# Performance work log

Hardware: AMD Instinct MI355X
Metric: run time of the kernel (lower is better)

The kernel has to match this reference:

```python
import jax, jax.numpy as jnp
import numpy as np

P, G, UV = 5, 40000, 256          # n_parts, gs_num (visible UV texels), uv_size
ZD, FD, HD = 32, 64, 32           # latent_z_dim, latent_f_dim, latent_h_dim
H1, L1 = 128, 3                   # mlp1 hidden dim, fc layers
H2, L2 = 128, 3                   # mlp2 hidden dim, fc layers
CC, LC = 64, 4                    # cnn hidden channels, cnn hidden layers


def _mlp_params(key, din, hid, nlayers, dout, nparts):
    ks = jax.random.split(key, 3)
    s = lambda f: 1.0 / np.sqrt(f)
    return dict(
        w_in=jax.random.normal(ks[0], (nparts, din, hid), jnp.float32) * s(din),
        b_in=jnp.zeros((nparts, hid), jnp.float32),
        w_hid=jax.random.normal(ks[1], (nparts, nlayers - 1, hid, hid), jnp.float32) * s(hid),
        b_hid=jnp.zeros((nparts, nlayers - 1, hid), jnp.float32),
        w_out=jax.random.normal(ks[2], (nparts, hid, dout), jnp.float32) * s(hid),
        b_out=jnp.zeros((nparts, dout), jnp.float32),
    )


def setup_inputs() -> dict:
    key = jax.random.key(0)
    ks = jax.random.split(key, 12)
    d1 = FD + ZD
    d2 = d1 + 3 + 11
    inp = {
        'latent_z': jax.random.normal(ks[2], (G, ZD), jnp.float32),
        'latent_f': jax.random.normal(ks[3], (P, FD), jnp.float32),
        'cano_xyz': jax.random.normal(ks[4], (G, 3), jnp.float32),
    }
    for k, v in _mlp_params(ks[0], d1, H1, L1, 11, P).items():
        inp['mlp1_' + k] = v
    for k, v in _mlp_params(ks[1], d2, H2, L2, HD, P).items():
        inp['mlp2_' + k] = v
    inp['conv_in_w'] = jax.random.normal(ks[5], (CC, HD, 3, 3), jnp.float32) * (1.0 / np.sqrt(HD * 9))
    inp['conv_in_b'] = jnp.zeros((CC,), jnp.float32)
    inp['conv_hid_w'] = jax.random.normal(ks[6], (LC - 1, CC, CC, 3, 3), jnp.float32) * (1.0 / np.sqrt(CC * 9))
    inp['conv_hid_b'] = jnp.zeros((LC - 1, CC), jnp.float32)
    inp['conv_out_w'] = jax.random.normal(ks[7], (3, CC, 3, 3), jnp.float32) * (1.0 / np.sqrt(CC * 9))
    inp['conv_out_b'] = jnp.zeros((3,), jnp.float32)
    inp['gs_part'] = jax.random.randint(ks[8], (G,), 0, P, jnp.int32)
    inp['uv_idx'] = jax.random.permutation(ks[9], UV * UV)[:G].astype(jnp.int32)  # unique visible texels
    return inp


def _part_mlp(x, w_in, b_in, w_hid, b_hid, w_out, b_out, part):
    # x: [G, D]; weights stacked over parts. Run every part's MLP, gather by part id.
    h = jax.nn.leaky_relu(jnp.einsum('gd,pdh->pgh', x, w_in) + b_in[:, None, :])
    for l in range(w_hid.shape[1]):
        h = jax.nn.leaky_relu(jnp.einsum('pgh,pho->pgo', h, w_hid[:, l]) + b_hid[:, l][:, None, :])
    out = jnp.einsum('pgh,pho->pgo', h, w_out) + b_out[:, None, :]  # [P, G, O]
    return out[part, jnp.arange(out.shape[1])]                       # [G, O]


def _conv(x, w, b):
    y = jax.lax.conv_general_dilated(x, w, (1, 1), 'SAME',
                                     dimension_numbers=('NCHW', 'OIHW', 'NCHW'))
    return y + b[None, :, None, None]


def _instance_norm(x, eps=1e-5):
    m = x.mean(axis=(2, 3), keepdims=True)
    v = x.var(axis=(2, 3), keepdims=True)
    return (x - m) / jnp.sqrt(v + eps)


def reference(latent_z, latent_f, cano_xyz,
              mlp1_w_in, mlp1_b_in, mlp1_w_hid, mlp1_b_hid, mlp1_w_out, mlp1_b_out,
              mlp2_w_in, mlp2_b_in, mlp2_w_hid, mlp2_b_hid, mlp2_w_out, mlp2_b_out,
              conv_in_w, conv_in_b, conv_hid_w, conv_hid_b, conv_out_w, conv_out_b,
              gs_part, uv_idx):
    feat_f = latent_f[gs_part]                                  # [G, FD] per-part feature gather
    x1 = jnp.concatenate([feat_f, latent_z], axis=-1)           # [G, FD+ZD]
    attrs = _part_mlp(x1, mlp1_w_in, mlp1_b_in, mlp1_w_hid, mlp1_b_hid,
                      mlp1_w_out, mlp1_b_out, gs_part)          # [G, 11] gaussian attrs
    x2 = jnp.concatenate([x1, cano_xyz, attrs], axis=-1)        # [G, FD+ZD+3+11]
    h = _part_mlp(x2, mlp2_w_in, mlp2_b_in, mlp2_w_hid, mlp2_b_hid,
                  mlp2_w_out, mlp2_b_out, gs_part)              # [G, HD]
    # scatter per-gaussian features back into the UV map (uvmask-indexed texels)
    uvmap = jnp.zeros((UV * UV, h.shape[-1]), h.dtype).at[uv_idx].add(h)
    x = uvmap.T.reshape(1, h.shape[-1], UV, UV)                 # [1, HD, UV, UV]
    # CNN refinement: conv -> (relu, conv, instance_norm) x (LC-1) -> conv -> sigmoid
    x = _conv(x, conv_in_w, conv_in_b)
    for l in range(conv_hid_w.shape[0]):
        x = _instance_norm(_conv(jax.nn.relu(x), conv_hid_w[l], conv_hid_b[l]))
    x = _conv(x, conv_out_w, conv_out_b)
    return jax.nn.sigmoid(x)                                    # [1, 3, UV, UV]
```

## Files before the change

kernel.cpp:

```cpp
#include <hip/hip_runtime.h>

#define G_N 40000
#define P_N 5
#define PIX 65536
#define XP 136
#define SP 40

typedef short short8 __attribute__((ext_vector_type(8)));
typedef short short4v __attribute__((ext_vector_type(4)));
typedef float f32x4 __attribute__((ext_vector_type(4)));
#define MFMA16(a, b, c) __builtin_amdgcn_mfma_f32_16x16x32_bf16(a, b, c, 0, 0, 0)

__device__ __forceinline__ short f2b(float f) {
    unsigned u = __builtin_bit_cast(unsigned, f);
    unsigned r = (u + 0x7fffu + ((u >> 16) & 1u)) >> 16;
    return (short)r;
}
__device__ __forceinline__ float b2f(short s) {
    unsigned u = ((unsigned)(unsigned short)s) << 16;
    return __builtin_bit_cast(float, u);
}


__global__ __launch_bounds__(256) void hist_k(const int* __restrict__ part,
                                              int* __restrict__ counts, int n) {
    __shared__ int s_c[P_N];
    if (threadIdx.x < P_N) s_c[threadIdx.x] = 0;
    __syncthreads();
    int g = blockIdx.x * 256 + threadIdx.x;
    if (g < n) atomicAdd(&s_c[part[g]], 1);
    __syncthreads();
    if (threadIdx.x < P_N) atomicAdd(&counts[threadIdx.x], s_c[threadIdx.x]);
}

__global__ void offs_k(const int* __restrict__ counts, int* __restrict__ offs) {
    if (threadIdx.x == 0) {
        int o = 0;
        for (int p = 0; p < P_N; ++p) {
            offs[p] = o;
            o += (counts[p] + 63) & ~63;
        }
        offs[P_N] = o;
    }
}

__global__ __launch_bounds__(256) void scatter_k(const int* __restrict__ part,
                                                 const int* __restrict__ offs,
                                                 int* __restrict__ cursors,
                                                 int* __restrict__ perm, int n) {
    const int t = threadIdx.x;
    const int g = blockIdx.x * 256 + t;
    const int p = (g < n) ? part[g] : -1;
    const int lane = t & 63;
    const int wid = t >> 6;
    __shared__ int s_wc[4][P_N];
    __shared__ int s_base[P_N];
    const unsigned long long lmask = (1ull << lane) - 1ull;
    int myrank = 0;
    for (int pp = 0; pp < P_N; ++pp) {
        unsigned long long m = __ballot(p == pp);
        if (p == pp) myrank = __popcll(m & lmask);
        if (lane == 0) s_wc[wid][pp] = __popcll(m);
    }
    __syncthreads();
    if (t < P_N) {
        int tot = s_wc[0][t] + s_wc[1][t] + s_wc[2][t] + s_wc[3][t];
        s_base[t] = atomicAdd(&cursors[t], tot);
    }
    __syncthreads();
    if (g < n) {
        int pre = 0;
        #pragma unroll
        for (int w2 = 0; w2 < 4; ++w2) if (w2 < wid) pre += s_wc[w2][p];
        perm[offs[p] + s_base[p] + pre + myrank] = g;
    }
}


__device__ __forceinline__ float mseg(int l, const float* __restrict__ src,
                                      int DIN, int DOUT, int NP, int pps) {
    const int pn = NP * 128;
    const int p = l / pn;
    const int r = l - p * pn;
    const int n = r >> 7, k = r & 127;
    return (n < DOUT && k < DIN) ? src[p * pps + k * DOUT + n] : 0.f;
}
__device__ __forceinline__ float cseg(int l, const float* __restrict__ src, int CIN) {
    const int per = 9 * 64 * CIN;
    const int ll = l / per;
    int rem = l - ll * per;
    const int tap = rem / (64 * CIN);
    rem -= tap * 64 * CIN;
    const int och = rem / CIN;
    const int ci = rem - och * CIN;
    return src[((ll * 64 + och) * CIN + ci) * 9 + tap];
}

__global__ __launch_bounds__(256) void prep_k(
        const float* __restrict__ m1wi, const float* __restrict__ m1wh,
        const float* __restrict__ m1wo, const float* __restrict__ m2wi,
        const float* __restrict__ m2wh, const float* __restrict__ m2wo,
        const float* __restrict__ cinw, const float* __restrict__ chw,
        short* __restrict__ wb) {
    const int idx = blockIdx.x * 256 + threadIdx.x;
    if (idx >= 651264) return;
    float v;
    if      (idx < 81920)  v = mseg(idx,          m1wi,         96, 128, 128, 12288);
    else if (idx < 163840) v = mseg(idx - 81920,  m1wh,        128, 128, 128, 32768);
    else if (idx < 245760) v = mseg(idx - 163840, m1wh + 16384,128, 128, 128, 32768);
    else if (idx < 256000) v = mseg(idx - 245760, m1wo,        128,  11,  16, 1408);
    else if (idx < 337920) v = mseg(idx - 256000, m2wi,        110, 128, 128, 14080);
    else if (idx < 419840) v = mseg(idx - 337920, m2wh,        128, 128, 128, 32768);
    else if (idx < 501760) v = mseg(idx - 419840, m2wh + 16384,128, 128, 128, 32768);
    else if (idx < 522240) v = mseg(idx - 501760, m2wo,        128,  32,  32, 4096);
    else if (idx < 540672) v = cseg(idx - 522240, cinw, 32);
    else                   v = cseg(idx - 540672, chw, 64);
    wb[idx] = f2b(v);
}


template<int NKC, bool ACT>
__device__ __forceinline__ void wcompute(const short8 (&A)[4][NKC],
                                         const short* __restrict__ wt,
                                         const float* __restrict__ bias,
                                         short* dst) {
    const int ln = threadIdx.x & 15, lq = threadIdx.x >> 4;
    #pragma unroll
    for (int nt = 0; nt < 8; ++nt) {
        short8 B[NKC];
        #pragma unroll
        for (int kc = 0; kc < NKC; ++kc)
            B[kc] = *(const short8*)(wt + (nt * 16 + ln) * 128 + kc * 32 + lq * 8);
        const float bs = bias[nt * 16 + ln];
        #pragma unroll
        for (int mt = 0; mt < 4; ++mt) {
            f32x4 acc = {bs, bs, bs, bs};
            #pragma unroll
            for (int kc = 0; kc < NKC; ++kc) acc = MFMA16(A[mt][kc], B[kc], acc);
            #pragma unroll
            for (int r = 0; r < 4; ++r) {
                float v = acc[r];
                if (ACT) v = fmaxf(v, 0.01f * v);
                dst[(mt * 16 + lq * 4 + r) * XP + nt * 16 + ln] = f2b(v);
            }
        }
    }
}

__device__ __forceinline__ void preload4(short8 (&A)[4][4], const short* s) {
    const int ln = threadIdx.x & 15, lq = threadIdx.x >> 4;
    #pragma unroll
    for (int mt = 0; mt < 4; ++mt)
        #pragma unroll
        for (int kc = 0; kc < 4; ++kc)
            A[mt][kc] = *(const short8*)(s + (mt * 16 + ln) * XP + kc * 32 + lq * 8);
}

__global__ __launch_bounds__(64, 2) void mlp_k(
        const float* __restrict__ latent_z, const float* __restrict__ latent_f,
        const float* __restrict__ cano,
        const short* __restrict__ wt1i, const float* __restrict__ b1i,
        const short* __restrict__ wt1h0, const short* __restrict__ wt1h1,
        const float* __restrict__ b1h,
        const short* __restrict__ wt1o, const float* __restrict__ b1o,
        const short* __restrict__ wt2i, const float* __restrict__ b2i,
        const short* __restrict__ wt2h0, const short* __restrict__ wt2h1,
        const float* __restrict__ b2h,
        const short* __restrict__ wt2o, const float* __restrict__ b2o,
        const int* __restrict__ uv_idx, const int* __restrict__ perm,
        const int* __restrict__ offs, const int* __restrict__ counts,
        unsigned short* __restrict__ uvmap ) {
    __shared__ short s_h[64 * XP];
    __shared__ short s_c4[64 * SP];
    __shared__ int s_g[64];
    __shared__ int s_uv[64];

    const int t = threadIdx.x;
    const int ln = t & 15, lq = t >> 4;
    const int pos0 = blockIdx.x * 64;
    if (pos0 >= offs[P_N]) return;
    int p = 0;
    #pragma unroll
    for (int q = 1; q < P_N; ++q) if (pos0 >= offs[q]) p = q;
    const int vend = offs[p] + counts[p];

    {
        const int pos = pos0 + t;
        const int g = (pos < vend) ? perm[pos] : -1;
        s_g[t] = g;
        s_uv[t] = (g >= 0) ? uv_idx[g] : 0;
    }
    for (int i = t; i < 64 * SP / 2; i += 64) ((int*)s_c4)[i] = 0;
    __syncthreads();

    for (int i = t; i < 64 * 16; i += 64) {
        const int g = i >> 4, k4 = (i & 15) * 4;
        const float4 v = *(const float4*)(latent_f + p * 64 + k4);
        short4v o = {f2b(v.x), f2b(v.y), f2b(v.z), f2b(v.w)};
        *(short4v*)(s_h + g * XP + k4) = o;
    }
    for (int i = t; i < 64 * 8; i += 64) {
        const int g = i >> 3, k4 = (i & 7) * 4;
        const int gg = s_g[g];
        short4v o = {0, 0, 0, 0};
        if (gg >= 0) {
            const float4 v = *(const float4*)(latent_z + gg * 32 + k4);
            o[0] = f2b(v.x); o[1] = f2b(v.y); o[2] = f2b(v.z); o[3] = f2b(v.w);
        }
        *(short4v*)(s_h + g * XP + 64 + k4) = o;
    }
    for (int i = t; i < 64 * 3; i += 64) {
        const int g = i / 3, k = i - g * 3;
        const int gg = s_g[g];
        s_c4[g * SP + k] = (gg >= 0) ? f2b(cano[gg * 3 + k]) : 0;
    }
    __syncthreads();

    short8 A1[4][3];
    #pragma unroll
    for (int mt = 0; mt < 4; ++mt)
        #pragma unroll
        for (int kc = 0; kc < 3; ++kc)
            A1[mt][kc] = *(const short8*)(s_h + (mt * 16 + ln) * XP + kc * 32 + lq * 8);
    __syncthreads();

    wcompute<3, true>(A1, wt1i + p * 16384, b1i + p * 128, s_h);
    __syncthreads();
    {
        short8 Ah[4][4];
        preload4(Ah, s_h); __syncthreads();
        wcompute<4, true>(Ah, wt1h0 + p * 16384, b1h + (p * 2 + 0) * 128, s_h);
        __syncthreads();
        preload4(Ah, s_h); __syncthreads();
        wcompute<4, true>(Ah, wt1h1 + p * 16384, b1h + (p * 2 + 1) * 128, s_h);
        __syncthreads();
        preload4(Ah, s_h); __syncthreads();
        short8 B[4];
        #pragma unroll
        for (int kc = 0; kc < 4; ++kc)
            B[kc] = *(const short8*)(wt1o + p * 2048 + ln * 128 + kc * 32 + lq * 8);
        const float bs = (ln < 11) ? b1o[p * 11 + ln] : 0.f;
        #pragma unroll
        for (int mt = 0; mt < 4; ++mt) {
            f32x4 acc = {bs, bs, bs, bs};
            #pragma unroll
            for (int kc = 0; kc < 4; ++kc) acc = MFMA16(Ah[mt][kc], B[kc], acc);
            if (ln < 11) {
                #pragma unroll
                for (int r = 0; r < 4; ++r)
                    s_c4[(mt * 16 + lq * 4 + r) * SP + 3 + ln] = f2b(acc[r]);
            }
        }
    }
    __syncthreads();

    {
        short8 A2[4][4];
        #pragma unroll
        for (int mt = 0; mt < 4; ++mt) {
            A2[mt][0] = A1[mt][0]; A2[mt][1] = A1[mt][1]; A2[mt][2] = A1[mt][2];
            A2[mt][3] = *(const short8*)(s_c4 + (mt * 16 + ln) * SP + lq * 8);
        }
        __syncthreads();
        wcompute<4, true>(A2, wt2i + p * 16384, b2i + p * 128, s_h);
    }
    __syncthreads();
    {
        short8 Ah[4][4];
        preload4(Ah, s_h); __syncthreads();
        wcompute<4, true>(Ah, wt2h0 + p * 16384, b2h + (p * 2 + 0) * 128, s_h);
        __syncthreads();
        preload4(Ah, s_h); __syncthreads();
        wcompute<4, true>(Ah, wt2h1 + p * 16384, b2h + (p * 2 + 1) * 128, s_h);
        __syncthreads();
        preload4(Ah, s_h);
        #pragma unroll
        for (int nt = 0; nt < 2; ++nt) {
            short8 B[4];
            #pragma unroll
            for (int kc = 0; kc < 4; ++kc)
                B[kc] = *(const short8*)(wt2o + p * 4096 + (nt * 16 + ln) * 128 + kc * 32 + lq * 8);
            const float bs = b2o[p * 32 + nt * 16 + ln];
            #pragma unroll
            for (int mt = 0; mt < 4; ++mt) {
                f32x4 acc = {bs, bs, bs, bs};
                #pragma unroll
                for (int kc = 0; kc < 4; ++kc) acc = MFMA16(Ah[mt][kc], B[kc], acc);
                #pragma unroll
                for (int r = 0; r < 4; ++r) {
                    const int m = mt * 16 + lq * 4 + r;
                    const int g = s_g[m];
                    if (g >= 0)
                        uvmap[s_uv[m] * 32 + nt * 16 + ln] = (unsigned short)f2b(acc[r]);
                }
            }
        }
    }
}


template<int CIN, int TRANS, bool STATS>
__global__ __launch_bounds__(128, 2) void conv_k(
        const unsigned short* __restrict__ in,
        const short* __restrict__ wt,
        const float* __restrict__ bias,
        const float* __restrict__ psum, const float* __restrict__ psq,
        unsigned short* __restrict__ out,
        float* __restrict__ ssum, float* __restrict__ ssq) {
    constexpr int CS = CIN + 8;
    constexpr int NKC = CIN / 32;
    constexpr int RUNS = CIN / 8;
    __shared__ short s_in[10 * 18 * CS];
    __shared__ float s_mr[2][64];
    __shared__ float s_red[2][2][64];

    const int t = threadIdx.x;
    const int ln = t & 15, lq = (t >> 4) & 3;
    const int w2 = t >> 6;
    const int tx0 = blockIdx.x * 16, ty0 = blockIdx.y * 8;

    if (TRANS == 2 && t < 64) {
        const float m = psum[t] * (1.f / PIX);
        const float vv = psq[t] * (1.f / PIX) - m * m;
        s_mr[0][t] = m;
        s_mr[1][t] = rsqrtf(vv + 1e-5f);
    }
    if (TRANS == 2) __syncthreads();

    for (int i = t; i < 180 * RUNS; i += 128) {
        const int sp = i / RUNS, run = i - sp * RUNS;
        const int r = sp / 18, c = sp - r * 18;
        const int gy = ty0 + r - 1, gx = tx0 + c - 1;
        short* dst = &s_in[(r * 18 + c) * CS + run * 8];
        if (gy >= 0 && gy < 256 && gx >= 0 && gx < 256) {
            short8 v = *(const short8*)(in + ((gy * 256 + gx) * CIN + run * 8));
            if (TRANS == 0) {
                *(short8*)dst = v;
            } else {
                short8 o;
                #pragma unroll
                for (int j = 0; j < 8; ++j) {
                    float f = b2f(v[j]);
                    if (TRANS == 2) f = (f - s_mr[0][run * 8 + j]) * s_mr[1][run * 8 + j];
                    o[j] = f2b(fmaxf(f, 0.f));
                }
                *(short8*)dst = o;
            }
        } else {
            short8 z = {0, 0, 0, 0, 0, 0, 0, 0};
            *(short8*)dst = z;
        }
    }
    __syncthreads();

    f32x4 acc[4][4];
    {
        float bs[4];
        #pragma unroll
        for (int nt = 0; nt < 4; ++nt) bs[nt] = bias[nt * 16 + ln];
        #pragma unroll
        for (int mt = 0; mt < 4; ++mt)
            #pragma unroll
            for (int nt = 0; nt < 4; ++nt) {
                f32x4 a = {bs[nt], bs[nt], bs[nt], bs[nt]};
                acc[mt][nt] = a;
            }
    }

    #pragma unroll
    for (int tap = 0; tap < 9; ++tap) {
        const int dy = tap / 3, dx = tap - dy * 3;
        const short* wtap = wt + tap * 64 * CIN;
        #pragma unroll
        for (int kc = 0; kc < NKC; ++kc) {
            short8 B[4];
            #pragma unroll
            for (int nt = 0; nt < 4; ++nt)
                B[nt] = *(const short8*)(wtap + (nt * 16 + ln) * CIN + kc * 32 + lq * 8);
            short8 A[4];
            #pragma unroll
            for (int mt = 0; mt < 4; ++mt)
                A[mt] = *(const short8*)&s_in[((w2 * 4 + mt + dy) * 18 + ln + dx) * CS + kc * 32 + lq * 8];
            #pragma unroll
            for (int mt = 0; mt < 4; ++mt)
                #pragma unroll
                for (int nt = 0; nt < 4; ++nt)
                    acc[mt][nt] = MFMA16(A[mt], B[nt], acc[mt][nt]);
        }
    }

    #pragma unroll
    for (int nt = 0; nt < 4; ++nt) {
        float ls = 0.f, lsq = 0.f;
        #pragma unroll
        for (int mt = 0; mt < 4; ++mt) {
            const int gy = ty0 + w2 * 4 + mt;
            #pragma unroll
            for (int r = 0; r < 4; ++r) {
                const float v = acc[mt][nt][r];
                const int gx = tx0 + lq * 4 + r;
                out[(gy * 256 + gx) * 64 + nt * 16 + ln] = (unsigned short)f2b(v);
                if (STATS) { ls += v; lsq = fmaf(v, v, lsq); }
            }
        }
        if (STATS) {
            ls  += __shfl_xor(ls, 16, 64);
            ls  += __shfl_xor(ls, 32, 64);
            lsq += __shfl_xor(lsq, 16, 64);
            lsq += __shfl_xor(lsq, 32, 64);
            if (lq == 0 && (t & 32) == 0) {
                s_red[w2][0][nt * 16 + ln] = ls;
                s_red[w2][1][nt * 16 + ln] = lsq;
            }
        }
    }
    if (STATS) {
        __syncthreads();
        if (t < 64) {
            atomicAdd(&ssum[t], s_red[0][0][t] + s_red[1][0][t]);
            atomicAdd(&ssq[t],  s_red[0][1][t] + s_red[1][1][t]);
        }
    }
}

__global__ __launch_bounds__(128) void convout_k(
        const unsigned short* __restrict__ in,
        const float* __restrict__ w,
        const float* __restrict__ bias,
        const float* __restrict__ psum, const float* __restrict__ psq,
        float* __restrict__ out) {
    constexpr int CS = 72;
    __shared__ short s_in[10 * 18 * CS];
    __shared__ float s_w[3][9][64];
    __shared__ float s_mr[2][64];

    const int t = threadIdx.x;
    const int tx0 = blockIdx.x * 16, ty0 = blockIdx.y * 8;
    if (t < 64) {
        const float m = psum[t] * (1.f / PIX);
        const float vv = psq[t] * (1.f / PIX) - m * m;
        s_mr[0][t] = m;
        s_mr[1][t] = rsqrtf(vv + 1e-5f);
    }
    __syncthreads();

    for (int i = t; i < 180 * 8; i += 128) {
        const int sp = i >> 3, run = i & 7;
        const int r = sp / 18, c = sp - r * 18;
        const int gy = ty0 + r - 1, gx = tx0 + c - 1;
        short* dst = &s_in[(r * 18 + c) * CS + run * 8];
        if (gy >= 0 && gy < 256 && gx >= 0 && gx < 256) {
            short8 v = *(const short8*)(in + ((gy * 256 + gx) * 64 + run * 8));
            short8 o;
            #pragma unroll
            for (int j = 0; j < 8; ++j) {
                const float f = (b2f(v[j]) - s_mr[0][run * 8 + j]) * s_mr[1][run * 8 + j];
                o[j] = f2b(f);
            }
            *(short8*)dst = o;
        } else {
            short8 z = {0, 0, 0, 0, 0, 0, 0, 0};
            *(short8*)dst = z;
        }
    }
    for (int i = t; i < 1728; i += 128) {
        const int o = i / 576;
        const int rem = i - o * 576;
        const int tap = rem >> 6;
        const int ci = rem & 63;
        s_w[o][tap][ci] = w[o * 576 + ci * 9 + tap];
    }
    __syncthreads();

    const int py = t >> 4, px = t & 15;
    float a0 = bias[0], a1 = bias[1], a2 = bias[2];
    for (int tap = 0; tap < 9; ++tap) {
        const int dy = tap / 3, dx = tap % 3;
        const short* rp = &s_in[((py + dy) * 18 + (px + dx)) * CS];
        #pragma unroll
        for (int c8 = 0; c8 < 8; ++c8) {
            short8 v = *(const short8*)(rp + c8 * 8);
            #pragma unroll
            for (int j = 0; j < 8; ++j) {
                const float f = b2f(v[j]);
                const int ci = c8 * 8 + j;
                a0 = fmaf(f, s_w[0][tap][ci], a0);
                a1 = fmaf(f, s_w[1][tap][ci], a1);
                a2 = fmaf(f, s_w[2][tap][ci], a2);
            }
        }
    }
    const int pix = (ty0 + py) * 256 + tx0 + px;
    out[pix]           = 1.f / (1.f + expf(-a0));
    out[PIX + pix]     = 1.f / (1.f + expf(-a1));
    out[2 * PIX + pix] = 1.f / (1.f + expf(-a2));
}


extern "C" void kernel_launch(void* const* d_in, const int* in_sizes, int n_in,
                              void* d_out, int out_size, void* d_ws, size_t ws_size,
                              hipStream_t stream) {
    (void)in_sizes; (void)n_in; (void)out_size; (void)ws_size;
    const float* latent_z = (const float*)d_in[0];
    const float* latent_f = (const float*)d_in[1];
    const float* cano     = (const float*)d_in[2];
    const float* m1wi = (const float*)d_in[3];
    const float* m1bi = (const float*)d_in[4];
    const float* m1wh = (const float*)d_in[5];
    const float* m1bh = (const float*)d_in[6];
    const float* m1wo = (const float*)d_in[7];
    const float* m1bo = (const float*)d_in[8];
    const float* m2wi = (const float*)d_in[9];
    const float* m2bi = (const float*)d_in[10];
    const float* m2wh = (const float*)d_in[11];
    const float* m2bh = (const float*)d_in[12];
    const float* m2wo = (const float*)d_in[13];
    const float* m2bo = (const float*)d_in[14];
    const float* cinw = (const float*)d_in[15];
    const float* cinb = (const float*)d_in[16];
    const float* chw  = (const float*)d_in[17];
    const float* chb  = (const float*)d_in[18];
    const float* cow  = (const float*)d_in[19];
    const float* cob  = (const float*)d_in[20];
    const int* gs_part = (const int*)d_in[21];
    const int* uv_idx  = (const int*)d_in[22];

    float* ws = (float*)d_ws;
    unsigned short* actA = (unsigned short*)ws;
    unsigned short* actB = (unsigned short*)(ws + 2097152);
    unsigned short* uvmap = actB;

    short* wb = (short*)(ws + 4194304);
    short* wt1i  = wb;
    short* wt1h0 = wb + 81920;
    short* wt1h1 = wb + 163840;
    short* wt1o  = wb + 245760;
    short* wt2i  = wb + 256000;
    short* wt2h0 = wb + 337920;
    short* wt2h1 = wb + 419840;
    short* wt2o  = wb + 501760;
    short* cwt_in  = wb + 522240;
    short* cwt_hid = wb + 540672;

    float* small = ws + 4194304 + 330000;
    int* counts  = (int*)small;
    int* cursors = counts + 8;
    int* offs    = cursors + 8;
    float* ssum  = small + 32;
    float* ssq   = ssum + 192;
    int* perm    = (int*)(ssq + 192);

    hipMemsetAsync(uvmap, 0, (size_t)PIX * 32 * sizeof(unsigned short), stream);
    hipMemsetAsync(small, 0, 1024 * sizeof(float), stream);

    hist_k<<<157, 256, 0, stream>>>(gs_part, counts, G_N);
    offs_k<<<1, 64, 0, stream>>>(counts, offs);
    scatter_k<<<157, 256, 0, stream>>>(gs_part, offs, cursors, perm, G_N);

    prep_k<<<2544, 256, 0, stream>>>(m1wi, m1wh, m1wo, m2wi, m2wh, m2wo, cinw, chw, wb);

    mlp_k<<<630, 64, 0, stream>>>(latent_z, latent_f, cano,
        wt1i, m1bi, wt1h0, wt1h1, m1bh, wt1o, m1bo,
        wt2i, m2bi, wt2h0, wt2h1, m2bh, wt2o, m2bo,
        uv_idx, perm, offs, counts, uvmap);

    dim3 cgrid(16, 32);
    conv_k<32, 0, false><<<cgrid, 128, 0, stream>>>(uvmap, cwt_in, cinb,
        nullptr, nullptr, actA, nullptr, nullptr);
    conv_k<64, 1, true><<<cgrid, 128, 0, stream>>>(actA, cwt_hid, chb,
        nullptr, nullptr, actB, ssum, ssq);
    conv_k<64, 2, true><<<cgrid, 128, 0, stream>>>(actB, cwt_hid + 36864, chb + 64,
        ssum, ssq, actA, ssum + 64, ssq + 64);
    conv_k<64, 2, true><<<cgrid, 128, 0, stream>>>(actA, cwt_hid + 73728, chb + 128,
        ssum + 64, ssq + 64, actB, ssum + 128, ssq + 128);
    convout_k<<<cgrid, 128, 0, stream>>>(actB, cow, cob,
        ssum + 128, ssq + 128, (float*)d_out);
}
```

Before: 262.8 us.

## Split MLP and conv tiles across more waves, drop MLP block barriers

The MLP kernel now uses two wavefronts per 64-gaussian block. Each wave owns 32 rows of the shared activation buffer, so the per-layer __syncthreads between layers go away. The conv kernels move from 128 to 256 threads, and each wave computes two output rows instead of four. Each wave also preloads all weight fragments for a tap before its MFMA loop. This gives more waves per tile for latency hiding and shorter dependent chains, at the cost of more register pressure from the hoisted B fragments and more redundant weight loads per block.

New measurement: 283.5 us. 1.08x slower.

```diff
diff --git a/kernel.cpp b/kernel.cpp
--- a/kernel.cpp
+++ b/kernel.cpp
@@ -4,7 +4,7 @@
 #define P_N 5
 #define PIX 65536
 #define XP 136
-#define SP 40
+#define SP 32
 
 typedef short short8 __attribute__((ext_vector_type(8)));
 typedef short short4v __attribute__((ext_vector_type(4)));
@@ -120,11 +120,10 @@
 
 
 template<int NKC, bool ACT>
-__device__ __forceinline__ void wcompute(const short8 (&A)[4][NKC],
+__device__ __forceinline__ void wlayer32(const short8 (&A)[2][NKC],
                                          const short* __restrict__ wt,
                                          const float* __restrict__ bias,
-                                         short* dst) {
-    const int ln = threadIdx.x & 15, lq = threadIdx.x >> 4;
+                                         short* dst, int ln, int lq) {
     #pragma unroll
     for (int nt = 0; nt < 8; ++nt) {
         short8 B[NKC];
@@ -133,7 +132,7 @@
             B[kc] = *(const short8*)(wt + (nt * 16 + ln) * 128 + kc * 32 + lq * 8);
         const float bs = bias[nt * 16 + ln];
         #pragma unroll
-        for (int mt = 0; mt < 4; ++mt) {
+        for (int mt = 0; mt < 2; ++mt) {
             f32x4 acc = {bs, bs, bs, bs};
             #pragma unroll
             for (int kc = 0; kc < NKC; ++kc) acc = MFMA16(A[mt][kc], B[kc], acc);
@@ -147,16 +146,15 @@
     }
 }
 
-__device__ __forceinline__ void preload4(short8 (&A)[4][4], const short* s) {
-    const int ln = threadIdx.x & 15, lq = threadIdx.x >> 4;
+__device__ __forceinline__ void pre2(short8 (&A)[2][4], const short* s, int ln, int lq) {
     #pragma unroll
-    for (int mt = 0; mt < 4; ++mt)
+    for (int mt = 0; mt < 2; ++mt)
         #pragma unroll
         for (int kc = 0; kc < 4; ++kc)
             A[mt][kc] = *(const short8*)(s + (mt * 16 + ln) * XP + kc * 32 + lq * 8);
 }
 
-__global__ __launch_bounds__(64, 2) void mlp_k(
+__global__ __launch_bounds__(128, 2) void mlp_k(
         const float* __restrict__ latent_z, const float* __restrict__ latent_f,
         const float* __restrict__ cano,
         const short* __restrict__ wt1i, const float* __restrict__ b1i,
@@ -176,7 +174,9 @@
     __shared__ int s_uv[64];
 
     const int t = threadIdx.x;
-    const int ln = t & 15, lq = t >> 4;
+    const int lane = t & 63;
+    const int ln = lane & 15, lq = lane >> 4;
+    const int w = t >> 6;
     const int pos0 = blockIdx.x * 64;
     if (pos0 >= offs[P_N]) return;
     int p = 0;
@@ -184,22 +184,22 @@
     for (int q = 1; q < P_N; ++q) if (pos0 >= offs[q]) p = q;
     const int vend = offs[p] + counts[p];
 
-    {
+    if (t < 64) {
         const int pos = pos0 + t;
         const int g = (pos < vend) ? perm[pos] : -1;
         s_g[t] = g;
         s_uv[t] = (g >= 0) ? uv_idx[g] : 0;
     }
-    for (int i = t; i < 64 * SP / 2; i += 64) ((int*)s_c4)[i] = 0;
-    __syncthreads();
-
-    for (int i = t; i < 64 * 16; i += 64) {
+    for (int i = t; i < 64 * SP / 2; i += 128) ((int*)s_c4)[i] = 0;
+    __syncthreads();
+
+    for (int i = t; i < 64 * 16; i += 128) {
         const int g = i >> 4, k4 = (i & 15) * 4;
         const float4 v = *(const float4*)(latent_f + p * 64 + k4);
         short4v o = {f2b(v.x), f2b(v.y), f2b(v.z), f2b(v.w)};
         *(short4v*)(s_h + g * XP + k4) = o;
     }
-    for (int i = t; i < 64 * 8; i += 64) {
+    for (int i = t; i < 64 * 8; i += 128) {
         const int g = i >> 3, k4 = (i & 7) * 4;
         const int gg = s_g[g];
         short4v o = {0, 0, 0, 0};
@@ -209,71 +209,66 @@
         }
         *(short4v*)(s_h + g * XP + 64 + k4) = o;
     }
-    for (int i = t; i < 64 * 3; i += 64) {
+    for (int i = t; i < 64 * 3; i += 128) {
         const int g = i / 3, k = i - g * 3;
         const int gg = s_g[g];
         s_c4[g * SP + k] = (gg >= 0) ? f2b(cano[gg * 3 + k]) : 0;
     }
     __syncthreads();
 
-    short8 A1[4][3];
+    short* myh = s_h + w * 32 * XP;
+    short* myc = s_c4 + w * 32 * SP;
+    const int gbase = w * 32;
+
+    short8 A1[2][3];
     #pragma unroll
-    for (int mt = 0; mt < 4; ++mt)
+    for (int mt = 0; mt < 2; ++mt)
         #pragma unroll
         for (int kc = 0; kc < 3; ++kc)
-            A1[mt][kc] = *(const short8*)(s_h + (mt * 16 + ln) * XP + kc * 32 + lq * 8);
-    __syncthreads();
-
-    wcompute<3, true>(A1, wt1i + p * 16384, b1i + p * 128, s_h);
-    __syncthreads();
+            A1[mt][kc] = *(const short8*)(myh + (mt * 16 + ln) * XP + kc * 32 + lq * 8);
+
+    wlayer32<3, true>(A1, wt1i + p * 16384, b1i + p * 128, myh, ln, lq);
     {
-        short8 Ah[4][4];
-        preload4(Ah, s_h); __syncthreads();
-        wcompute<4, true>(Ah, wt1h0 + p * 16384, b1h + (p * 2 + 0) * 128, s_h);
-        __syncthreads();
-        preload4(Ah, s_h); __syncthreads();
-        wcompute<4, true>(Ah, wt1h1 + p * 16384, b1h + (p * 2 + 1) * 128, s_h);
-        __syncthreads();
-        preload4(Ah, s_h); __syncthreads();
+        short8 Ah[2][4];
+        pre2(Ah, myh, ln, lq);
+        wlayer32<4, true>(Ah, wt1h0 + p * 16384, b1h + (p * 2 + 0) * 128, myh, ln, lq);
+        pre2(Ah, myh, ln, lq);
+        wlayer32<4, true>(Ah, wt1h1 + p * 16384, b1h + (p * 2 + 1) * 128, myh, ln, lq);
+        pre2(Ah, myh, ln, lq);
         short8 B[4];
         #pragma unroll
         for (int kc = 0; kc < 4; ++kc)
             B[kc] = *(const short8*)(wt1o + p * 2048 + ln * 128 + kc * 32 + lq * 8);
         const float bs = (ln < 11) ? b1o[p * 11 + ln] : 0.f;
         #pragma unroll
-        for (int mt = 0; mt < 4; ++mt) {
+        for (int mt = 0; mt < 2; ++mt) {
             f32x4 acc = {bs, bs, bs, bs};
             #pragma unroll
             for (int kc = 0; kc < 4; ++kc) acc = MFMA16(Ah[mt][kc], B[kc], acc);
             if (ln < 11) {
                 #pragma unroll
                 for (int r = 0; r < 4; ++r)
-                    s_c4[(mt * 16 + lq * 4 + r) * SP + 3 + ln] = f2b(acc[r]);
-            }
-        }
-    }
-    __syncthreads();
+                    myc[(mt * 16 + lq * 4 + r) * SP + 3 + ln] = f2b(acc[r]);
+            }
+        }
+    }
 
     {
-        short8 A2[4][4];
-        #pragma unroll
-        for (int mt = 0; mt < 4; ++mt) {
+        short8 A2[2][4];
+        #pragma unroll
+        for (int mt = 0; mt < 2; ++mt) {
             A2[mt][0] = A1[mt][0]; A2[mt][1] = A1[mt][1]; A2[mt][2] = A1[mt][2];
-            A2[mt][3] = *(const short8*)(s_c4 + (mt * 16 + ln) * SP + lq * 8);
-        }
-        __syncthreads();
-        wcompute<4, true>(A2, wt2i + p * 16384, b2i + p * 128, s_h);
-    }
-    __syncthreads();
+            A2[mt][3] = *(const short8*)(myc + (mt * 16 + ln) * SP + lq * 8);
+        }
+        wlayer32<4, true>(A2, wt2i + p * 16384, b2i + p * 128, myh, ln, lq);
+    }
     {
-        short8 Ah[4][4];
-        preload4(Ah, s_h); __syncthreads();
-        wcompute<4, true>(Ah, wt2h0 + p * 16384, b2h + (p * 2 + 0) * 128, s_h);
-        __syncthreads();
-        preload4(Ah, s_h); __syncthreads();
-        wcompute<4, true>(Ah, wt2h1 + p * 16384, b2h + (p * 2 + 1) * 128, s_h);
-        __syncthreads();
-        preload4(Ah, s_h);
+        short8 Ah[2][4];
+        pre2(Ah, myh, ln, lq);
+        wlayer32<4, true>(Ah, wt2h0 + p * 16384, b2h + (p * 2 + 0) * 128, myh, ln, lq);
+        pre2(Ah, myh, ln, lq);
+        wlayer32<4, true>(Ah, wt2h1 + p * 16384, b2h + (p * 2 + 1) * 128, myh, ln, lq);
+        pre2(Ah, myh, ln, lq);
         #pragma unroll
         for (int nt = 0; nt < 2; ++nt) {
             short8 B[4];
@@ -282,15 +277,14 @@
                 B[kc] = *(const short8*)(wt2o + p * 4096 + (nt * 16 + ln) * 128 + kc * 32 + lq * 8);
             const float bs = b2o[p * 32 + nt * 16 + ln];
             #pragma unroll
-            for (int mt = 0; mt < 4; ++mt) {
+            for (int mt = 0; mt < 2; ++mt) {
                 f32x4 acc = {bs, bs, bs, bs};
                 #pragma unroll
                 for (int kc = 0; kc < 4; ++kc) acc = MFMA16(Ah[mt][kc], B[kc], acc);
                 #pragma unroll
                 for (int r = 0; r < 4; ++r) {
-                    const int m = mt * 16 + lq * 4 + r;
-                    const int g = s_g[m];
-                    if (g >= 0)
+                    const int m = gbase + mt * 16 + lq * 4 + r;
+                    if (s_g[m] >= 0)
                         uvmap[s_uv[m] * 32 + nt * 16 + ln] = (unsigned short)f2b(acc[r]);
                 }
             }
@@ -300,7 +294,7 @@
 
 
 template<int CIN, int TRANS, bool STATS>
-__global__ __launch_bounds__(128, 2) void conv_k(
+__global__ __launch_bounds__(256, 2) void conv_k(
         const unsigned short* __restrict__ in,
         const short* __restrict__ wt,
         const float* __restrict__ bias,
@@ -312,11 +306,12 @@
     constexpr int RUNS = CIN / 8;
     __shared__ short s_in[10 * 18 * CS];
     __shared__ float s_mr[2][64];
-    __shared__ float s_red[2][2][64];
+    __shared__ float s_red[4][2][64];
 
     const int t = threadIdx.x;
-    const int ln = t & 15, lq = (t >> 4) & 3;
-    const int w2 = t >> 6;
+    const int lane = t & 63;
+    const int ln = lane & 15, lq = lane >> 4;
+    const int w4 = t >> 6;
     const int tx0 = blockIdx.x * 16, ty0 = blockIdx.y * 8;
 
     if (TRANS == 2 && t < 64) {
@@ -327,7 +322,7 @@
     }
     if (TRANS == 2) __syncthreads();
 
-    for (int i = t; i < 180 * RUNS; i += 128) {
+    for (int i = t; i < 180 * RUNS; i += 256) {
         const int sp = i / RUNS, run = i - sp * RUNS;
         const int r = sp / 18, c = sp - r * 18;
         const int gy = ty0 + r - 1, gx = tx0 + c - 1;
@@ -353,13 +348,13 @@
     }
     __syncthreads();
 
-    f32x4 acc[4][4];
+    f32x4 acc[2][4];
     {
         float bs[4];
         #pragma unroll
         for (int nt = 0; nt < 4; ++nt) bs[nt] = bias[nt * 16 + ln];
         #pragma unroll
-        for (int mt = 0; mt < 4; ++mt)
+        for (int mt = 0; mt < 2; ++mt)
             #pragma unroll
             for (int nt = 0; nt < 4; ++nt) {
                 f32x4 a = {bs[nt], bs[nt], bs[nt], bs[nt]};
@@ -367,25 +362,28 @@
             }
     }
 
+    const int r0 = w4 * 2;
     #pragma unroll
     for (int tap = 0; tap < 9; ++tap) {
         const int dy = tap / 3, dx = tap - dy * 3;
         const short* wtap = wt + tap * 64 * CIN;
+        short8 Bc[NKC][4];
+        #pragma unroll
+        for (int kc = 0; kc < NKC; ++kc)
+            #pragma unroll
+            for (int nt = 0; nt < 4; ++nt)
+                Bc[kc][nt] = *(const short8*)(wtap + (nt * 16 + ln) * CIN + kc * 32 + lq * 8);
         #pragma unroll
         for (int kc = 0; kc < NKC; ++kc) {
-            short8 B[4];
-            #pragma unroll
-            for (int nt = 0; nt < 4; ++nt)
-                B[nt] = *(const short8*)(wtap + (nt * 16 + ln) * CIN + kc * 32 + lq * 8);
-            short8 A[4];
-            #pragma unroll
-            for (int mt = 0; mt < 4; ++mt)
-                A[mt] = *(const short8*)&s_in[((w2 * 4 + mt + dy) * 18 + ln + dx) * CS + kc * 32 + lq * 8];
-            #pragma unroll
-            for (int mt = 0; mt < 4; ++mt)
+            short8 A[2];
+            #pragma unroll
+            for (int mt = 0; mt < 2; ++mt)
+                A[mt] = *(const short8*)&s_in[((r0 + mt + dy) * 18 + ln + dx) * CS + kc * 32 + lq * 8];
+            #pragma unroll
+            for (int mt = 0; mt < 2; ++mt)
                 #pragma unroll
                 for (int nt = 0; nt < 4; ++nt)
-                    acc[mt][nt] = MFMA16(A[mt], B[nt], acc[mt][nt]);
+                    acc[mt][nt] = MFMA16(A[mt], Bc[kc][nt], acc[mt][nt]);
         }
     }
 
@@ -393,8 +391,8 @@
     for (int nt = 0; nt < 4; ++nt) {
         float ls = 0.f, lsq = 0.f;
         #pragma unroll
-        for (int mt = 0; mt < 4; ++mt) {
-            const int gy = ty0 + w2 * 4 + mt;
+        for (int mt = 0; mt < 2; ++mt) {
+            const int gy = ty0 + r0 + mt;
             #pragma unroll
             for (int r = 0; r < 4; ++r) {
                 const float v = acc[mt][nt][r];
@@ -408,17 +406,17 @@
             ls  += __shfl_xor(ls, 32, 64);
             lsq += __shfl_xor(lsq, 16, 64);
             lsq += __shfl_xor(lsq, 32, 64);
-            if (lq == 0 && (t & 32) == 0) {
-                s_red[w2][0][nt * 16 + ln] = ls;
-                s_red[w2][1][nt * 16 + ln] = lsq;
+            if (lane < 16) {
+                s_red[w4][0][nt * 16 + ln] = ls;
+                s_red[w4][1][nt * 16 + ln] = lsq;
             }
         }
     }
     if (STATS) {
         __syncthreads();
         if (t < 64) {
-            atomicAdd(&ssum[t], s_red[0][0][t] + s_red[1][0][t]);
-            atomicAdd(&ssq[t],  s_red[0][1][t] + s_red[1][1][t]);
+            atomicAdd(&ssum[t], s_red[0][0][t] + s_red[1][0][t] + s_red[2][0][t] + s_red[3][0][t]);
+            atomicAdd(&ssq[t],  s_red[0][1][t] + s_red[1][1][t] + s_red[2][1][t] + s_red[3][1][t]);
         }
     }
 }
@@ -559,19 +557,19 @@
 
     prep_k<<<2544, 256, 0, stream>>>(m1wi, m1wh, m1wo, m2wi, m2wh, m2wo, cinw, chw, wb);
 
-    mlp_k<<<630, 64, 0, stream>>>(latent_z, latent_f, cano,
+    mlp_k<<<630, 128, 0, stream>>>(latent_z, latent_f, cano,
         wt1i, m1bi, wt1h0, wt1h1, m1bh, wt1o, m1bo,
         wt2i, m2bi, wt2h0, wt2h1, m2bh, wt2o, m2bo,
         uv_idx, perm, offs, counts, uvmap);
 
     dim3 cgrid(16, 32);
-    conv_k<32, 0, false><<<cgrid, 128, 0, stream>>>(uvmap, cwt_in, cinb,
+    conv_k<32, 0, false><<<cgrid, 256, 0, stream>>>(uvmap, cwt_in, cinb,
         nullptr, nullptr, actA, nullptr, nullptr);
-    conv_k<64, 1, true><<<cgrid, 128, 0, stream>>>(actA, cwt_hid, chb,
+    conv_k<64, 1, true><<<cgrid, 256, 0, stream>>>(actA, cwt_hid, chb,
         nullptr, nullptr, actB, ssum, ssq);
-    conv_k<64, 2, true><<<cgrid, 128, 0, stream>>>(actB, cwt_hid + 36864, chb + 64,
+    conv_k<64, 2, true><<<cgrid, 256, 0, stream>>>(actB, cwt_hid + 36864, chb + 64,
         ssum, ssq, actA, ssum + 64, ssq + 64);
-    conv_k<64, 2, true><<<cgrid, 128, 0, stream>>>(actA, cwt_hid + 73728, chb + 128,
+    conv_k<64, 2, true><<<cgrid, 256, 0, stream>>>(actA, cwt_hid + 73728, chb + 128,
         ssum + 64, ssq + 64, actB, ssum + 128, ssq + 128);
     convout_k<<<cgrid, 128, 0, stream>>>(actB, cow, cob,
         ssum + 128, ssq + 128, (float*)d_out);
```
